# Optimization experiments

Hardware: AMD Instinct MI355X
Metric: run time of the kernel (lower is better)

## Reference

```python
import jax, jax.numpy as jnp
import numpy as np

N, E, D = 50000, 800000, 128
EPS = 1e-5  # PyG BatchNorm default eps


def setup_inputs() -> dict:
    key = jax.random.key(0)
    ks = jax.random.split(key, 12)
    s = 1.0 / np.sqrt(D)
    x = jax.random.normal(ks[0], (N, D), jnp.float32)
    edge_index = jax.random.randint(ks[1], (2, E), 0, N, dtype=jnp.int32)
    Wp = jax.random.normal(ks[2], (D, D), jnp.float32) * s
    bp = jax.random.normal(ks[3], (D,), jnp.float32) * 0.01
    # 4 SAGEConv layers, all 128->128, stacked: lin_l (neighbor, with bias) and lin_r (root)
    Wl = jax.random.normal(ks[4], (4, D, D), jnp.float32) * s
    bl = jax.random.normal(ks[5], (4, D), jnp.float32) * 0.01
    Wr = jax.random.normal(ks[6], (4, D, D), jnp.float32) * s
    # BatchNorm params/buffers (eval mode: running stats)
    bn_gamma = 1.0 + 0.1 * jax.random.normal(ks[7], (4, D), jnp.float32)
    bn_beta = 0.1 * jax.random.normal(ks[8], (4, D), jnp.float32)
    bn_mean = 0.1 * jax.random.normal(ks[9], (4, D), jnp.float32)
    bn_var = jax.random.uniform(ks[10], (4, D), jnp.float32, 0.5, 1.5)
    return {"x": x, "edge_index": edge_index, "Wp": Wp, "bp": bp, "Wl": Wl,
            "bl": bl, "Wr": Wr, "bn_gamma": bn_gamma, "bn_beta": bn_beta,
            "bn_mean": bn_mean, "bn_var": bn_var}


def _sage_conv(x, src, dst, inv_deg, Wl, bl, Wr):
    # mean-aggregate neighbor features: gather x[src], scatter-sum to dst, divide by degree
    agg = jax.ops.segment_sum(x[src], dst, num_segments=N) * inv_deg  # [N, D]
    # PyG SAGEConv: lin_l(aggr) + lin_r(x_root)
    return agg @ Wl + bl + x @ Wr


def _bn(h, gamma, beta, mean, var):
    return (h - mean) * (gamma * jax.lax.rsqrt(var + EPS)) + beta


def reference(x, edge_index, Wp, bp, Wl, bl, Wr, bn_gamma, bn_beta, bn_mean, bn_var):
    src, dst = edge_index[0], edge_index[1]
    deg = jax.ops.segment_sum(jnp.ones((E,), x.dtype), dst, num_segments=N)
    inv_deg = (1.0 / jnp.maximum(deg, 1.0))[:, None]  # [N, 1]
    x = jax.nn.relu(x @ Wp + bp)
    # eval mode: dropout is identity, BN uses running stats
    for i in range(3):
        h = _sage_conv(x, src, dst, inv_deg, Wl[i], bl[i], Wr[i])
        h = jax.nn.relu(_bn(h, bn_gamma[i], bn_beta[i], bn_mean[i], bn_var[i]))
        x = x + h
    x = _sage_conv(x, src, dst, inv_deg, Wl[3], bl[3], Wr[3])
    return jax.nn.relu(_bn(x, bn_gamma[3], bn_beta[3], bn_mean[3], bn_var[3]))
```

## Files before the change

kernel.cpp:

```cpp
#include <hip/hip_runtime.h>

#define DIM 128
#define BN_EPS 1e-5f
#define BCAP 8192
#define EPB 4096
#define EPT 16

typedef __bf16 bf16x8 __attribute__((ext_vector_type(8)));
typedef float f32x4 __attribute__((ext_vector_type(4)));

__device__ __forceinline__ float bf_e0(unsigned int u) {
    return __builtin_bit_cast(float, u << 16);
}
__device__ __forceinline__ float bf_e1(unsigned int u) {
    return __builtin_bit_cast(float, u & 0xffff0000u);
}
__device__ __forceinline__ unsigned short f2b(float f) {
    __bf16 b = (__bf16)f;
    return __builtin_bit_cast(unsigned short, b);
}
__device__ __forceinline__ unsigned int pack2(float lo, float hi) {
    return (unsigned int)f2b(lo) | ((unsigned int)f2b(hi) << 16);
}

__global__ __launch_bounds__(256) void k_bin(const int* __restrict__ src,
                                             const int* __restrict__ dst,
                                             int* __restrict__ cursor,
                                             unsigned int* __restrict__ binned,
                                             int E, int NB) {
    __shared__ int hist[256];
    __shared__ int base[256];
    __shared__ int c2[256];
    const int tid = threadIdx.x;
    const int e0 = blockIdx.x * EPB;

    unsigned int u[EPT];
    int b[EPT];
    hist[tid] = 0;
    c2[tid] = 0;
    __syncthreads();
#pragma unroll
    for (int i = 0; i < EPT; ++i) {
        int e = e0 + i * 256 + tid;
        if (e < E) {
            int d = dst[e];
            b[i] = d >> 8;
            u[i] = ((unsigned int)(d & 255) << 17) | (unsigned int)src[e];
            atomicAdd(&hist[b[i]], 1);
        } else {
            b[i] = -1;
        }
    }
    __syncthreads();
    if (tid < NB && hist[tid] > 0) base[tid] = atomicAdd(&cursor[tid], hist[tid]);
    __syncthreads();
#pragma unroll
    for (int i = 0; i < EPT; ++i) {
        if (b[i] < 0) continue;
        int p = base[b[i]] + atomicAdd(&c2[b[i]], 1);
        if (p < BCAP) binned[(size_t)b[i] * BCAP + p] = u[i];
    }
}

__global__ __launch_bounds__(256) void k_bscan(const int* __restrict__ cursor,
                                               int* __restrict__ bbase,
                                               int* __restrict__ rowptr, int NB,
                                               int N, int E) {
    __shared__ int sh[256];
    int t = threadIdx.x;
    int v = (t < NB) ? min(cursor[t], BCAP) : 0;
    sh[t] = v;
    __syncthreads();
    for (int off = 1; off < 256; off <<= 1) {
        int a = (t >= off) ? sh[t - off] : 0;
        __syncthreads();
        sh[t] += a;
        __syncthreads();
    }
    if (t < NB) bbase[t] = sh[t] - v;
    if (t == 0) rowptr[N] = E;
}

__global__ __launch_bounds__(256) void k_csr(const int* __restrict__ cursor,
                                             const int* __restrict__ bbase,
                                             const unsigned int* __restrict__ binned,
                                             int* __restrict__ rowptr,
                                             float* __restrict__ inv_deg,
                                             int* __restrict__ col, int N) {
    __shared__ unsigned int stage[BCAP];
    __shared__ int deg[256];
    __shared__ int start[256];
    const int b = blockIdx.x;
    const int t = threadIdx.x;
    const int node0 = b << 8;
    const int cnt = min(cursor[b], BCAP);
    const int gbase = bbase[b];

    deg[t] = 0;
    __syncthreads();
    for (int e = t; e < cnt; e += 256) {
        unsigned int u = binned[(size_t)b * BCAP + e];
        stage[e] = u;
        atomicAdd(&deg[u >> 17], 1);
    }
    __syncthreads();
    int d = deg[t];
    start[t] = d;
    __syncthreads();
    for (int off = 1; off < 256; off <<= 1) {
        int a = (t >= off) ? start[t - off] : 0;
        __syncthreads();
        start[t] += a;
        __syncthreads();
    }
    int excl = start[t] - d;
    int node = node0 + t;
    if (node < N) {
        rowptr[node] = gbase + excl;
        inv_deg[node] = 1.0f / (float)(d > 1 ? d : 1);
    }
    __syncthreads();
    deg[t] = excl;
    __syncthreads();
    for (int e = t; e < cnt; e += 256) {
        unsigned int u = stage[e];
        int dl = u >> 17;
        int p = atomicAdd(&deg[dl], 1);
        col[gbase + p] = (int)(u & 0x1ffffu);
    }
}

__global__ void k_wtr(const float* __restrict__ Wp, const float* __restrict__ Wl,
                      const float* __restrict__ Wr, unsigned short* __restrict__ WTf) {
    int gid = blockIdx.x * blockDim.x + threadIdx.x;
    if (gid >= 9 * 2048) return;
    int m = gid >> 11;
    int r = gid & 2047;
    int lane = r & 63;
    int k = (r >> 6) & 3;
    int ct = r >> 8;
    int feat = ct * 16 + (lane & 15);
    int kb = k * 32 + (lane >> 4) * 8;
    const float* W = (m == 0) ? Wp : (m < 5) ? (Wl + (size_t)(m - 1) * DIM * DIM)
                                             : (Wr + (size_t)(m - 5) * DIM * DIM);
    unsigned short o[8];
#pragma unroll
    for (int e = 0; e < 8; ++e) o[e] = f2b(W[(size_t)(kb + e) * DIM + feat]);
    *(uint4*)(WTf + (size_t)gid * 8) = *(const uint4*)o;
}

__global__ void k_agg(const uint4* __restrict__ xb4, const int* __restrict__ rowptr,
                      const int* __restrict__ col, const float* __restrict__ inv_deg,
                      uint4* __restrict__ aggb4, int n) {
    int node = (blockIdx.x * blockDim.x + threadIdx.x) >> 6;
    int lane = threadIdx.x & 63;
    if (node >= n) return;
    const int e4 = lane >> 4, c16 = lane & 15;
    const int lo = rowptr[node], hi = rowptr[node + 1];

    float a0 = 0.f, a1 = 0.f, a2 = 0.f, a3 = 0.f,
          a4 = 0.f, a5 = 0.f, a6 = 0.f, a7 = 0.f;

    int idx = lo + e4;
    int s_pre = (idx < hi) ? col[idx] : -1;
    for (int j = lo; j < hi; j += 4) {
        int s = s_pre;
        int nidx = j + 4 + e4;
        s_pre = (nidx < hi) ? col[nidx] : -1;
        if (s >= 0) {
            uint4 v = xb4[(size_t)s * 16 + c16];
            a0 += bf_e0(v.x); a1 += bf_e1(v.x);
            a2 += bf_e0(v.y); a3 += bf_e1(v.y);
            a4 += bf_e0(v.z); a5 += bf_e1(v.z);
            a6 += bf_e0(v.w); a7 += bf_e1(v.w);
        }
    }
#define RED_(a) a += __shfl_xor(a, 16); a += __shfl_xor(a, 32);
    RED_(a0) RED_(a1) RED_(a2) RED_(a3) RED_(a4) RED_(a5) RED_(a6) RED_(a7)
#undef RED_
    float sc = inv_deg[node];
    uint4 o;
    o.x = pack2(a0 * sc, a1 * sc);
    o.y = pack2(a2 * sc, a3 * sc);
    o.z = pack2(a4 * sc, a5 * sc);
    o.w = pack2(a6 * sc, a7 * sc);
    if (lane < 16) aggb4[(size_t)node * 16 + c16] = o;
}

template <int NSEG, bool A0F32>
__global__ __launch_bounds__(256) void k_gemm(
    const void* __restrict__ A0v, const unsigned short* __restrict__ A1,
    const unsigned short* __restrict__ Wf0, const unsigned short* __restrict__ Wf1,
    const float* __restrict__ bias,
    const float* __restrict__ gamma, const float* __restrict__ beta,
    const float* __restrict__ mean, const float* __restrict__ var,
    const unsigned short* __restrict__ residb,
    float* __restrict__ out32, unsigned short* __restrict__ outb, int nrows) {
    __shared__ unsigned short wlds[16384];
    __shared__ float colp[2 * DIM];

    const int tid = threadIdx.x;
    const int lane = tid & 63;
    const int wave = tid >> 6;
    const int l15 = lane & 15;
    const int lhi = lane >> 4;
    const int node = blockIdx.x * 64 + wave * 16 + l15;
    const int arow = node < nrows ? node : nrows - 1;

    if (tid < DIM) {
        float sc, sh;
        if (gamma) {
            float s = gamma[tid] * rsqrtf(var[tid] + BN_EPS);
            sc = s;
            sh = (bias[tid] - mean[tid]) * s + beta[tid];
        } else {
            sc = 1.f;
            sh = bias[tid];
        }
        colp[tid * 2] = sc;
        colp[tid * 2 + 1] = sh;
    }

    f32x4 acc[8];
#pragma unroll
    for (int ct = 0; ct < 8; ++ct) acc[ct] = (f32x4){0.f, 0.f, 0.f, 0.f};

    {
        const uint4* g = (const uint4*)Wf0;
        uint4* l = (uint4*)wlds;
#pragma unroll
        for (int i = 0; i < 8; ++i) l[tid + i * 256] = g[tid + i * 256];
    }
    __syncthreads();

    {
        bf16x8 af[4];
        if (A0F32) {
            const float* a0 = (const float*)A0v + (size_t)arow * DIM + lhi * 8;
#pragma unroll
            for (int k = 0; k < 4; ++k) {
                float4 v0 = *(const float4*)(a0 + k * 32);
                float4 v1 = *(const float4*)(a0 + k * 32 + 4);
                bf16x8 f;
                f[0] = (__bf16)v0.x; f[1] = (__bf16)v0.y;
                f[2] = (__bf16)v0.z; f[3] = (__bf16)v0.w;
                f[4] = (__bf16)v1.x; f[5] = (__bf16)v1.y;
                f[6] = (__bf16)v1.z; f[7] = (__bf16)v1.w;
                af[k] = f;
            }
        } else {
            const unsigned short* a0 = (const unsigned short*)A0v + (size_t)arow * DIM + lhi * 8;
#pragma unroll
            for (int k = 0; k < 4; ++k) af[k] = *(const bf16x8*)(a0 + k * 32);
        }
#pragma unroll
        for (int k = 0; k < 4; ++k) {
            bf16x8 bw[8];
#pragma unroll
            for (int ct = 0; ct < 8; ++ct)
                bw[ct] = *(const bf16x8*)&wlds[((ct * 4 + k) * 64 + lane) * 8];
#pragma unroll
            for (int ct = 0; ct < 8; ++ct)
                acc[ct] = __builtin_amdgcn_mfma_f32_16x16x32_bf16(bw[ct], af[k],
                                                                  acc[ct], 0, 0, 0);
        }
    }

    if (NSEG == 2) {
        __syncthreads();
        {
            const uint4* g = (const uint4*)Wf1;
            uint4* l = (uint4*)wlds;
#pragma unroll
            for (int i = 0; i < 8; ++i) l[tid + i * 256] = g[tid + i * 256];
        }
        __syncthreads();
        bf16x8 af[4];
        const unsigned short* a1 = A1 + (size_t)arow * DIM + lhi * 8;
#pragma unroll
        for (int k = 0; k < 4; ++k) af[k] = *(const bf16x8*)(a1 + k * 32);
#pragma unroll
        for (int k = 0; k < 4; ++k) {
            bf16x8 bw[8];
#pragma unroll
            for (int ct = 0; ct < 8; ++ct)
                bw[ct] = *(const bf16x8*)&wlds[((ct * 4 + k) * 64 + lane) * 8];
#pragma unroll
            for (int ct = 0; ct < 8; ++ct)
                acc[ct] = __builtin_amdgcn_mfma_f32_16x16x32_bf16(bw[ct], af[k],
                                                                  acc[ct], 0, 0, 0);
        }
    } else {
        __syncthreads();
    }

    if (node < nrows) {
#pragma unroll
        for (int ct = 0; ct < 8; ++ct) {
            int c0 = ct * 16 + lhi * 4;
            float h[4];
#pragma unroll
            for (int j = 0; j < 4; ++j) {
                float2 p = *(const float2*)&colp[(c0 + j) * 2];
                h[j] = fmaxf(acc[ct][j] * p.x + p.y, 0.f);
            }
            size_t base = (size_t)node * DIM + c0;
            if (residb) {
                uint2 rv = *(const uint2*)(residb + base);
                h[0] += bf_e0(rv.x); h[1] += bf_e1(rv.x);
                h[2] += bf_e0(rv.y); h[3] += bf_e1(rv.y);
            }
            if (outb) {
                uint2 o;
                o.x = pack2(h[0], h[1]);
                o.y = pack2(h[2], h[3]);
                *(uint2*)(outb + base) = o;
            }
            if (out32)
                *(float4*)(out32 + base) = make_float4(h[0], h[1], h[2], h[3]);
        }
    }
}

extern "C" void kernel_launch(void* const* d_in, const int* in_sizes, int n_in,
                              void* d_out, int out_size, void* d_ws, size_t ws_size,
                              hipStream_t stream) {
    const float* x_in = (const float*)d_in[0];
    const int* ei     = (const int*)d_in[1];
    const float* Wp   = (const float*)d_in[2];
    const float* bp   = (const float*)d_in[3];
    const float* Wl   = (const float*)d_in[4];
    const float* bl   = (const float*)d_in[5];
    const float* Wr   = (const float*)d_in[6];
    const float* g    = (const float*)d_in[7];
    const float* be   = (const float*)d_in[8];
    const float* mu   = (const float*)d_in[9];
    const float* va   = (const float*)d_in[10];

    const int N = in_sizes[0] / DIM;
    const int E = in_sizes[1] / 2;
    const int* src = ei;
    const int* dst = ei + E;
    const int NB = (N + 255) >> 8;

    char* p = (char*)d_ws;
    auto alloc = [&](size_t bytes) {
        char* r = p;
        p += (bytes + 255) & ~(size_t)255;
        return r;
    };
    float* inv_deg = (float*)alloc((size_t)N * 4);
    int* rowptr    = (int*)alloc((size_t)(N + 1) * 4);
    int* cursor    = (int*)alloc((size_t)NB * 4);
    int* bbase     = (int*)alloc((size_t)NB * 4);
    int* col       = (int*)alloc((size_t)E * 4);
    unsigned int* binned = (unsigned int*)alloc((size_t)NB * BCAP * 4);
    unsigned short* xb   = (unsigned short*)alloc((size_t)N * DIM * 2);
    unsigned short* aggb = (unsigned short*)alloc((size_t)N * DIM * 2);
    unsigned short* WTf  = (unsigned short*)alloc((size_t)9 * 16384 * 2);

    hipMemsetAsync(cursor, 0, (size_t)NB * 4, stream);
    k_bin<<<(E + EPB - 1) / EPB, 256, 0, stream>>>(src, dst, cursor, binned, E, NB);
    k_bscan<<<1, 256, 0, stream>>>(cursor, bbase, rowptr, NB, N, E);
    k_csr<<<NB, 256, 0, stream>>>(cursor, bbase, binned, rowptr, inv_deg, col, N);

    k_wtr<<<(9 * 2048 + 255) / 256, 256, 0, stream>>>(Wp, Wl, Wr, WTf);

    const int gblocks = (N + 63) / 64;

    k_gemm<1, true><<<gblocks, 256, 0, stream>>>(
        x_in, nullptr, WTf, nullptr, bp,
        nullptr, nullptr, nullptr, nullptr, nullptr, nullptr, xb, N);

    float* out = (float*)d_out;
    for (int i = 0; i < 4; ++i) {
        k_agg<<<(N + 3) / 4, 256, 0, stream>>>((const uint4*)xb, rowptr, col,
                                               inv_deg, (uint4*)aggb, N);
        const unsigned short* WlF = WTf + (size_t)(1 + i) * 16384;
        const unsigned short* WrF = WTf + (size_t)(5 + i) * 16384;
        k_gemm<2, false><<<gblocks, 256, 0, stream>>>(
            aggb, xb, WlF, WrF, bl + i * DIM,
            g + i * DIM, be + i * DIM, mu + i * DIM, va + i * DIM,
            (i < 3) ? xb : nullptr,
            (i < 3) ? nullptr : out, (i < 3) ? xb : nullptr, N);
    }
}
```

Baseline: 249.2 us.

## Store node features in feature-chunked layout so each XCD gathers one chunk

```diff
diff --git a/kernel.cpp b/kernel.cpp
--- a/kernel.cpp
+++ b/kernel.cpp
@@ -5,6 +5,7 @@
 #define BCAP 8192
 #define EPB 4096
 #define EPT 16
+#define NCHUNK 8
 
 typedef __bf16 bf16x8 __attribute__((ext_vector_type(8)));
 typedef float f32x4 __attribute__((ext_vector_type(4)));
@@ -149,42 +150,48 @@
     *(uint4*)(WTf + (size_t)gid * 8) = *(const uint4*)o;
 }
 
-__global__ void k_agg(const uint4* __restrict__ xb4, const int* __restrict__ rowptr,
-                      const int* __restrict__ col, const float* __restrict__ inv_deg,
-                      uint4* __restrict__ aggb4, int n) {
-    int node = (blockIdx.x * blockDim.x + threadIdx.x) >> 6;
-    int lane = threadIdx.x & 63;
+__global__ __launch_bounds__(256) void k_aggc(
+    const unsigned short* __restrict__ xc, const int* __restrict__ rowptr,
+    const int* __restrict__ col, const float* __restrict__ inv_deg,
+    unsigned short* __restrict__ aggb, int n) {
+    const int c = blockIdx.x & 7;
+    const int nb = blockIdx.x >> 3;
+    const int wave = threadIdx.x >> 6;
+    const int lane = threadIdx.x & 63;
+    const int n4 = lane >> 4;
+    const int e4 = (lane >> 2) & 3;
+    const int f4 = lane & 3;
+    const int node = nb * 16 + wave * 4 + n4;
     if (node >= n) return;
-    const int e4 = lane >> 4, c16 = lane & 15;
+
     const int lo = rowptr[node], hi = rowptr[node + 1];
-
-    float a0 = 0.f, a1 = 0.f, a2 = 0.f, a3 = 0.f,
-          a4 = 0.f, a5 = 0.f, a6 = 0.f, a7 = 0.f;
-
+    const uint2* tab = (const uint2*)(xc + (size_t)c * n * 16);
+
+    float a0 = 0.f, a1 = 0.f, a2 = 0.f, a3 = 0.f;
     int idx = lo + e4;
     int s_pre = (idx < hi) ? col[idx] : -1;
     for (int j = lo; j < hi; j += 4) {
         int s = s_pre;
-        int nidx = j + 4 + e4;
-        s_pre = (nidx < hi) ? col[nidx] : -1;
+        int ni = j + 4 + e4;
+        s_pre = (ni < hi) ? col[ni] : -1;
         if (s >= 0) {
-            uint4 v = xb4[(size_t)s * 16 + c16];
-            a0 += bf_e0(v.x); a1 += bf_e1(v.x);
-            a2 += bf_e0(v.y); a3 += bf_e1(v.y);
-            a4 += bf_e0(v.z); a5 += bf_e1(v.z);
-            a6 += bf_e0(v.w); a7 += bf_e1(v.w);
-        }
-    }
-#define RED_(a) a += __shfl_xor(a, 16); a += __shfl_xor(a, 32);
-    RED_(a0) RED_(a1) RED_(a2) RED_(a3) RED_(a4) RED_(a5) RED_(a6) RED_(a7)
+            uint2 v = tab[(size_t)s * 4 + f4];
+            a0 += bf_e0(v.x);
+            a1 += bf_e1(v.x);
+            a2 += bf_e0(v.y);
+            a3 += bf_e1(v.y);
+        }
+    }
+#define RED_(a) a += __shfl_xor(a, 4); a += __shfl_xor(a, 8);
+    RED_(a0) RED_(a1) RED_(a2) RED_(a3)
 #undef RED_
-    float sc = inv_deg[node];
-    uint4 o;
-    o.x = pack2(a0 * sc, a1 * sc);
-    o.y = pack2(a2 * sc, a3 * sc);
-    o.z = pack2(a4 * sc, a5 * sc);
-    o.w = pack2(a6 * sc, a7 * sc);
-    if (lane < 16) aggb4[(size_t)node * 16 + c16] = o;
+    if (e4 == 0) {
+        float sc = inv_deg[node];
+        uint2 o;
+        o.x = pack2(a0 * sc, a1 * sc);
+        o.y = pack2(a2 * sc, a3 * sc);
+        *(uint2*)(aggb + (size_t)node * DIM + c * 16 + f4 * 4) = o;
+    }
 }
 
 template <int NSEG, bool A0F32>
@@ -276,9 +283,13 @@
         }
         __syncthreads();
         bf16x8 af[4];
-        const unsigned short* a1 = A1 + (size_t)arow * DIM + lhi * 8;
-#pragma unroll
-        for (int k = 0; k < 4; ++k) af[k] = *(const bf16x8*)(a1 + k * 32);
+#pragma unroll
+        for (int k = 0; k < 4; ++k) {
+            int fb = k * 32 + lhi * 8;
+            const unsigned short* p =
+                A1 + ((size_t)(fb >> 4) * nrows + arow) * 16 + (fb & 15);
+            af[k] = *(const bf16x8*)p;
+        }
 #pragma unroll
         for (int k = 0; k < 4; ++k) {
             bf16x8 bw[8];
@@ -304,9 +315,9 @@
                 float2 p = *(const float2*)&colp[(c0 + j) * 2];
                 h[j] = fmaxf(acc[ct][j] * p.x + p.y, 0.f);
             }
-            size_t base = (size_t)node * DIM + c0;
+            size_t coff = ((size_t)ct * nrows + node) * 16 + lhi * 4;
             if (residb) {
-                uint2 rv = *(const uint2*)(residb + base);
+                uint2 rv = *(const uint2*)(residb + coff);
                 h[0] += bf_e0(rv.x); h[1] += bf_e1(rv.x);
                 h[2] += bf_e0(rv.y); h[3] += bf_e1(rv.y);
             }
@@ -314,10 +325,11 @@
                 uint2 o;
                 o.x = pack2(h[0], h[1]);
                 o.y = pack2(h[2], h[3]);
-                *(uint2*)(outb + base) = o;
+                *(uint2*)(outb + coff) = o;
             }
             if (out32)
-                *(float4*)(out32 + base) = make_float4(h[0], h[1], h[2], h[3]);
+                *(float4*)(out32 + (size_t)node * DIM + c0) =
+                    make_float4(h[0], h[1], h[2], h[3]);
         }
     }
 }
@@ -367,6 +379,7 @@
     k_wtr<<<(9 * 2048 + 255) / 256, 256, 0, stream>>>(Wp, Wl, Wr, WTf);
 
     const int gblocks = (N + 63) / 64;
+    const int ablocks = ((N + 15) / 16) * NCHUNK;
 
     k_gemm<1, true><<<gblocks, 256, 0, stream>>>(
         x_in, nullptr, WTf, nullptr, bp,
@@ -374,8 +387,7 @@
 
     float* out = (float*)d_out;
     for (int i = 0; i < 4; ++i) {
-        k_agg<<<(N + 3) / 4, 256, 0, stream>>>((const uint4*)xb, rowptr, col,
-                                               inv_deg, (uint4*)aggb, N);
+        k_aggc<<<ablocks, 256, 0, stream>>>(xb, rowptr, col, inv_deg, aggb, N);
         const unsigned short* WlF = WTf + (size_t)(1 + i) * 16384;
         const unsigned short* WrF = WTf + (size_t)(5 + i) * 16384;
         k_gemm<2, false><<<gblocks, 256, 0, stream>>>(
```

Measured after the change: 321.3 us. 1.29x slower.
